# Kernel tuning notes

Hardware: AMD Instinct MI355X
Metric: run time of the kernel (lower is better)

## Reference

```python
import jax, jax.numpy as jnp
import numpy as np

B, L, C = 256, 256, 128
HID, H = 128, 4
D = HID // H            # 32
NUM_LAYERS = 2
NEG_SLOPE = 0.2
LN_EPS = 1e-5


def setup_inputs() -> dict:
    key = jax.random.key(0)
    ks = jax.random.split(key, 16)
    E = 4096
    x = jax.random.normal(ks[0], (B, L, C), dtype=jnp.float32)
    edge_index = jax.random.randint(ks[1], (2, E), 0, C, dtype=jnp.int64)
    s_in = 1.0 / np.sqrt(L)
    s_h = 1.0 / np.sqrt(HID)
    return {
        "x": x,
        "edge_index": edge_index,
        "emb_W": jax.random.normal(ks[2], (L, HID), jnp.float32) * s_in,
        "emb_b": jnp.zeros((HID,), jnp.float32),
        "lin_l_W": jax.random.normal(ks[3], (NUM_LAYERS, HID, HID), jnp.float32) * s_h,
        "lin_l_b": jnp.zeros((NUM_LAYERS, HID), jnp.float32),
        "lin_r_W": jax.random.normal(ks[4], (NUM_LAYERS, HID, HID), jnp.float32) * s_h,
        "lin_r_b": jnp.zeros((NUM_LAYERS, HID), jnp.float32),
        "att": jax.random.normal(ks[5], (NUM_LAYERS, H, D), jnp.float32) * (1.0 / np.sqrt(D)),
        "gat_bias": jnp.zeros((NUM_LAYERS, HID), jnp.float32),
        "ln_gamma": jnp.ones((NUM_LAYERS, HID), jnp.float32),
        "ln_beta": jnp.zeros((NUM_LAYERS, HID), jnp.float32),
        "proj_W": jax.random.normal(ks[6], (HID, L), jnp.float32) * s_h,
        "proj_b": jnp.zeros((L,), jnp.float32),
    }


def _batch_edges(edge_index):
    # replicate single-graph edges per batch sample with node offsets, then add self loops
    E = edge_index.shape[1]
    off = jnp.repeat(jnp.arange(B, dtype=edge_index.dtype) * C, E)
    src = jnp.tile(edge_index[0], B) + off
    dst = jnp.tile(edge_index[1], B) + off
    loop = jnp.arange(B * C, dtype=edge_index.dtype)
    return jnp.concatenate([src, loop]), jnp.concatenate([dst, loop])


def _layer_norm(x, g, b):
    mu = jnp.mean(x, axis=-1, keepdims=True)
    var = jnp.mean(jnp.square(x - mu), axis=-1, keepdims=True)
    return (x - mu) * jax.lax.rsqrt(var + LN_EPS) * g + b


def _gatv2(x, src, dst, Wl, bl, Wr, br, a, bias):
    N = x.shape[0]
    xl = (x @ Wl + bl).reshape(N, H, D)   # source-side transform
    xr = (x @ Wr + br).reshape(N, H, D)   # target-side transform
    e = jax.nn.leaky_relu(xl[src] + xr[dst], NEG_SLOPE)   # (E', H, D)
    logits = jnp.einsum('ehd,hd->eh', e, a)               # (E', H)
    m = jax.ops.segment_max(logits, dst, num_segments=N)
    p = jnp.exp(logits - m[dst])
    s = jax.ops.segment_sum(p, dst, num_segments=N)
    alpha = p / (s[dst] + 1e-16)
    out = jax.ops.segment_sum(xl[src] * alpha[:, :, None], dst, num_segments=N)
    return out.reshape(N, HID) + bias, alpha


def reference(x, edge_index, emb_W, emb_b, lin_l_W, lin_l_b, lin_r_W, lin_r_b,
              att, gat_bias, ln_gamma, ln_beta, proj_W, proj_b):
    src, dst = _batch_edges(edge_index)
    # (B, L, C) -> nodes are channels: (B*C, L) -> embed to HID
    h = x.transpose(0, 2, 1).reshape(B * C, L) @ emb_W + emb_b
    alpha = None
    for i in range(NUM_LAYERS):
        new_h, alpha = _gatv2(h, src, dst, lin_l_W[i], lin_l_b[i],
                              lin_r_W[i], lin_r_b[i], att[i], gat_bias[i])
        new_h = jax.nn.elu(new_h)
        h = h + new_h
        h = _layer_norm(h, ln_gamma[i], ln_beta[i])
        # dropout: eval mode, identity
    # attention map (to_dense_adj semantics: adj[b, src%C, dst%C] = mean_h(alpha), then transpose)
    b_idx = src // C
    dense = jnp.zeros((B, C, C), x.dtype).at[b_idx, src % C, dst % C].add(alpha.mean(axis=-1))
    attn_map = dense.transpose(0, 2, 1)
    out = (h @ proj_W + proj_b).reshape(B, C, L).transpose(0, 2, 1)  # (B, L, C)
    return out, attn_map
```

## Files before the change

### kernel.cpp

```cpp
#include <hip/hip_runtime.h>
#include <hip/hip_fp16.h>
#include <math.h>

#define BB 256
#define LL 256
#define CC 128
#define HIDD 128
#define HH 4
#define DD 32
#define EE 4096
#define NN (BB*CC)
#define NEG_SLOPE 0.2f
#define LN_EPS 1e-5f
#define DEGMAX 58
#define LOG2CAP 31
#define CSRSL 3840
#define ASLOT 4352
#define AEDGE 4224

typedef short bf16x8 __attribute__((ext_vector_type(8)));
typedef float f32x4 __attribute__((ext_vector_type(4)));

__device__ __forceinline__ float red64(float p) {
    p += __shfl_xor(p, 32);
    p += __shfl_xor(p, 16);
    p += __shfl_xor(p, 8);
    p += __shfl_xor(p, 4);
    p += __shfl_xor(p, 2);
    p += __shfl_xor(p, 1);
    return p;
}
__device__ __forceinline__ unsigned bfr(float f) {
    unsigned x = __float_as_uint(f);
    return (x + 0x7FFFu + ((x >> 16) & 1u)) >> 16;
}
__device__ __forceinline__ unsigned pack2(float a, float b) { return bfr(a) | (bfr(b) << 16); }
__device__ __forceinline__ float blo(unsigned u) { return __uint_as_float(u << 16); }
__device__ __forceinline__ float bhi(unsigned u) { return __uint_as_float(u & 0xFFFF0000u); }

__device__ __forceinline__ void stage_f32_rm(ushort* lds, const float* src, int ldm, int t) {
    #pragma unroll
    for (int i = 0; i < 8; ++i) {
        int flat = i*256 + t;
        int r = flat >> 4, c = flat & 15;
        const float* p = src + (size_t)r*ldm + c*8;
        float4 v0 = *(const float4*)p;
        float4 v1 = *(const float4*)(p + 4);
        uint4 pk;
        pk.x = pack2(v0.x, v0.y); pk.y = pack2(v0.z, v0.w);
        pk.z = pack2(v1.x, v1.y); pk.w = pack2(v1.z, v1.w);
        *(uint4*)&lds[((r*16) + (c ^ (r & 7)))*8] = pk;
    }
}
__device__ __forceinline__ void stage_bf16_rm(ushort* lds, const ushort* src, int ldm, int t) {
    #pragma unroll
    for (int i = 0; i < 8; ++i) {
        int flat = i*256 + t;
        int r = flat >> 4, c = flat & 15;
        uint4 pk = *(const uint4*)(src + (size_t)r*ldm + c*8);
        *(uint4*)&lds[((r*16) + (c ^ (r & 7)))*8] = pk;
    }
}
__device__ __forceinline__ void mfma_tile_128(const ushort* Als, const ushort* Bls,
                                              f32x4 acc[2][8], int w, int lane) {
    int mr = lane & 15, quad = lane >> 4;
    #pragma unroll
    for (int ks = 0; ks < 4; ++ks) {
        int ca = ks*4 + quad;
        bf16x8 a[2], b[8];
        #pragma unroll
        for (int mf = 0; mf < 2; ++mf) {
            int m = w*32 + mf*16 + mr;
            a[mf] = *(const bf16x8*)&Als[((m*16) + (ca ^ (m & 7)))*8];
        }
        #pragma unroll
        for (int nf = 0; nf < 8; ++nf) {
            int n = nf*16 + mr;
            b[nf] = *(const bf16x8*)&Bls[((n*16) + (ca ^ (n & 7)))*8];
        }
        #pragma unroll
        for (int mf = 0; mf < 2; ++mf)
            #pragma unroll
            for (int nf = 0; nf < 8; ++nf)
                acc[mf][nf] = __builtin_amdgcn_mfma_f32_16x16x32_bf16(a[mf], b[nf], acc[mf][nf], 0, 0, 0);
    }
}
#define ZERO_ACC(acc) { _Pragma("unroll") for (int i_=0;i_<2;++i_) { _Pragma("unroll") for (int j_=0;j_<8;++j_) acc[i_][j_] = (f32x4){0.f,0.f,0.f,0.f}; } }

__global__ __launch_bounds__(256) void prep_weights(const float* __restrict__ emb_W,
                                                    const float* __restrict__ lWl,
                                                    const float* __restrict__ lWr,
                                                    const float* __restrict__ pW,
                                                    ushort* __restrict__ WembT,
                                                    ushort* __restrict__ WlrT,
                                                    ushort* __restrict__ WpT) {
    int gid = blockIdx.x * 256 + threadIdx.x;
    float v[8];
    if (gid < 4096) {
        int f = gid >> 5, ch = gid & 31;
        #pragma unroll
        for (int j = 0; j < 8; ++j) v[j] = emb_W[(size_t)(ch*8 + j)*HIDD + f];
        uint4 pk; pk.x = pack2(v[0],v[1]); pk.y = pack2(v[2],v[3]);
        pk.z = pack2(v[4],v[5]); pk.w = pack2(v[6],v[7]);
        *(uint4*)&WembT[(size_t)f*LL + ch*8] = pk;
    } else if (gid < 12288) {
        int g = gid - 4096;
        int mat = g >> 11, f = (g >> 4) & 127, ch = g & 15;
        const float* src = ((mat & 1) ? lWr : lWl) + (size_t)(mat >> 1)*HIDD*HIDD;
        #pragma unroll
        for (int j = 0; j < 8; ++j) v[j] = src[(size_t)(ch*8 + j)*HIDD + f];
        uint4 pk; pk.x = pack2(v[0],v[1]); pk.y = pack2(v[2],v[3]);
        pk.z = pack2(v[4],v[5]); pk.w = pack2(v[6],v[7]);
        *(uint4*)&WlrT[(size_t)mat*HIDD*HIDD + (size_t)f*HIDD + ch*8] = pk;
    } else {
        int g = gid - 12288;
        int l = g >> 4, ch = g & 15;
        #pragma unroll
        for (int j = 0; j < 8; ++j) v[j] = pW[(size_t)(ch*8 + j)*LL + l];
        uint4 pk; pk.x = pack2(v[0],v[1]); pk.y = pack2(v[2],v[3]);
        pk.z = pack2(v[4],v[5]); pk.w = pack2(v[6],v[7]);
        *(uint4*)&WpT[(size_t)l*HIDD + ch*8] = pk;
    }
}

__global__ __launch_bounds__(256) void transpose_x(const float* __restrict__ x,
                                                   ushort* __restrict__ xbfT) {
    __shared__ float tile[CC][33];
    int b = blockIdx.y, l0 = blockIdx.x * 32;
    int t = threadIdx.x;
    #pragma unroll
    for (int i = 0; i < 4; ++i) {
        int flat = i*256 + t;
        int l = flat >> 5, c4 = flat & 31;
        float4 v = *(const float4*)&x[((size_t)b*LL + l0 + l)*CC + c4*4];
        tile[c4*4+0][l] = v.x; tile[c4*4+1][l] = v.y;
        tile[c4*4+2][l] = v.z; tile[c4*4+3][l] = v.w;
    }
    __syncthreads();
    #pragma unroll
    for (int i = 0; i < 2; ++i) {
        int flat = i*256 + t;
        int c = flat >> 2, ch = flat & 3;
        const float* p = &tile[c][ch*8];
        uint4 pk; pk.x = pack2(p[0],p[1]); pk.y = pack2(p[2],p[3]);
        pk.z = pack2(p[4],p[5]); pk.w = pack2(p[6],p[7]);
        *(uint4*)&xbfT[((size_t)b*CC + c)*LL + l0 + ch*8] = pk;
    }
}

__global__ __launch_bounds__(256) void build_csr(const int* __restrict__ edge,
                                                 int* __restrict__ csr_off,
                                                 int* __restrict__ csr_src) {
    __shared__ int cnt[CC];
    __shared__ int offs[CC+1];
    __shared__ int cur[CC];
    int t = threadIdx.x;
    if (t < CC) cnt[t] = 0;
    __syncthreads();
    for (int j = t; j < EE; j += 256) atomicAdd(&cnt[edge[EE + j]], 1);
    __syncthreads();
    if (t == 0) {
        int a = 0;
        for (int i = 0; i < CC; ++i) { offs[i] = a; a += cnt[i]; }
        offs[CC] = a;
    }
    __syncthreads();
    if (t < CC) cur[t] = offs[t];
    if (t <= CC) csr_off[t] = offs[t];
    __syncthreads();
    for (int j = t; j < EE; j += 256) {
        int pos = atomicAdd(&cur[edge[EE + j]], 1);
        csr_src[pos] = edge[j];
    }
}

__global__ __launch_bounds__(256) void embed_mfma(const ushort* __restrict__ xbfT,
                                                  const ushort* __restrict__ WembT,
                                                  const float* __restrict__ bias,
                                                  float* __restrict__ hout) {
    __shared__ __align__(16) ushort Als[128*16*8];
    __shared__ __align__(16) ushort Bls[128*16*8];
    int b = blockIdx.x;
    int t = threadIdx.x, lane = t & 63, w = t >> 6;
    f32x4 acc[2][8];
    ZERO_ACC(acc)
    #pragma unroll
    for (int kh = 0; kh < 2; ++kh) {
        if (kh) __syncthreads();
        stage_bf16_rm(Als, xbfT + (size_t)b*CC*LL + kh*128, LL, t);
        stage_bf16_rm(Bls, WembT + kh*128, LL, t);
        __syncthreads();
        mfma_tile_128(Als, Bls, acc, w, lane);
    }
    int mr = lane & 15, quad = lane >> 4;
    #pragma unroll
    for (int nf = 0; nf < 8; ++nf) {
        int f = nf*16 + mr;
        float bv = bias[f];
        #pragma unroll
        for (int mf = 0; mf < 2; ++mf)
            #pragma unroll
            for (int r = 0; r < 4; ++r) {
                int node = w*32 + mf*16 + quad*4 + r;
                hout[((size_t)b*CC + node)*HIDD + f] = acc[mf][nf][r] + bv;
            }
    }
}

__global__ __launch_bounds__(256) void lin_mfma(const float* __restrict__ hmat,
                                                const ushort* __restrict__ WlT,
                                                const ushort* __restrict__ WrT,
                                                const float* __restrict__ bl,
                                                const float* __restrict__ br,
                                                float* __restrict__ xlT,
                                                float* __restrict__ xrT) {
    __shared__ __align__(16) ushort Als[128*16*8];
    __shared__ __align__(16) ushort Bls[128*16*8];
    const ushort* W   = blockIdx.y ? WrT : WlT;
    const float* bias = blockIdx.y ? br : bl;
    float* out        = blockIdx.y ? xrT : xlT;
    int m0 = blockIdx.x * 128;
    int t = threadIdx.x, lane = t & 63, w = t >> 6;
    f32x4 acc[2][8];
    ZERO_ACC(acc)
    stage_f32_rm(Als, hmat + (size_t)m0*HIDD, HIDD, t);
    stage_bf16_rm(Bls, W, HIDD, t);
    __syncthreads();
    mfma_tile_128(Als, Bls, acc, w, lane);
    int mr = lane & 15, quad = lane >> 4;
    #pragma unroll
    for (int nf = 0; nf < 8; ++nf) {
        int f = nf*16 + mr;
        float bv = bias[f];
        int h = f >> 5, d = f & 31;
        #pragma unroll
        for (int mf = 0; mf < 2; ++mf)
            #pragma unroll
            for (int r = 0; r < 4; ++r) {
                int node = w*32 + mf*16 + quad*4 + r;
                out[(((size_t)blockIdx.x*HH + h)*CC + node)*DD + d] = acc[mf][nf][r] + bv;
            }
    }
}

__global__ __launch_bounds__(128) void gat_attn(const float* __restrict__ xlT,
                                                const float* __restrict__ xrT,
                                                const int* __restrict__ csr_off,
                                                const int* __restrict__ csr_src,
                                                const float* __restrict__ att,
                                                float* __restrict__ xagg,
                                                float* __restrict__ alpha_ws) {
    __shared__ __align__(16) uint2 xl4[8*129];
    __shared__ __half mylog[128*LOG2CAP];
    __shared__ unsigned char csr_s[CSRSL];
    int bid = blockIdx.x;
    int b = bid >> 3, h = (bid >> 1) & 3, half = bid & 1;
    int t = threadIdx.x;
    int dst = half*64 + (t >> 1), p = t & 1;

    const float* xl_g = xlT + ((size_t)b*HH + h)*CC*DD;
    #pragma unroll
    for (int i = 0; i < 8; ++i) {
        int flat = i*128 + t;
        int n = flat >> 3, c = flat & 7;
        float4 v = *(const float4*)&xl_g[(size_t)n*DD + c*4];
        xl4[c*129 + n] = make_uint2(pack2(v.x, v.y), pack2(v.z, v.w));
    }
    int rbase = csr_off[half*64];
    int rcnt  = csr_off[half*64 + 64] - rbase;
    if (rcnt > CSRSL) rcnt = CSRSL;
    for (int j = t; j < rcnt; j += 128)
        csr_s[j] = (unsigned char)csr_src[rbase + j];

    float att_r[32], r_r[32], q_r[32];
    const float* xr_g = xrT + (((size_t)b*HH + h)*CC + dst) * DD;
    #pragma unroll
    for (int c = 0; c < 8; ++c) {
        float4 xv = *(const float4*)&xr_g[c*4];
        float4 av = *(const float4*)&att[h*DD + c*4];
        att_r[c*4+0]=av.x; att_r[c*4+1]=av.y; att_r[c*4+2]=av.z; att_r[c*4+3]=av.w;
        r_r[c*4+0]=av.x*xv.x; r_r[c*4+1]=av.y*xv.y; r_r[c*4+2]=av.z*xv.z; r_r[c*4+3]=av.w*xv.w;
        q_r[c*4+0]=copysignf(0.4f,av.x); q_r[c*4+1]=copysignf(0.4f,av.y);
        q_r[c*4+2]=copysignf(0.4f,av.z); q_r[c*4+3]=copysignf(0.4f,av.w);
    }
    int base = csr_off[dst];
    int deg  = csr_off[dst+1] - base;
    if (deg > DEGMAX) deg = DEGMAX;
    int sbase = base - rbase;
    __syncthreads();

    __half* ml = &mylog[t*LOG2CAP];
    float m = -1e30f;
    int nv = 0;
    for (int vj = p; vj <= deg; vj += 2, ++nv) {
        int src = (vj < deg) ? (int)csr_s[sbase + vj] : dst;
        float a0=0.f, a1=0.f, a2=0.f, a3=0.f;
        #pragma unroll
        for (int q = 0; q < 8; ++q) {
            uint2 u = xl4[q*129 + src];
            float pp;
            pp = fmaf(att_r[4*q+0], blo(u.x), r_r[4*q+0]);
            a0 = fmaf(0.6f, pp, a0); a0 = fmaf(q_r[4*q+0], fabsf(pp), a0);
            pp = fmaf(att_r[4*q+1], bhi(u.x), r_r[4*q+1]);
            a1 = fmaf(0.6f, pp, a1); a1 = fmaf(q_r[4*q+1], fabsf(pp), a1);
            pp = fmaf(att_r[4*q+2], blo(u.y), r_r[4*q+2]);
            a2 = fmaf(0.6f, pp, a2); a2 = fmaf(q_r[4*q+2], fabsf(pp), a2);
            pp = fmaf(att_r[4*q+3], bhi(u.y), r_r[4*q+3]);
            a3 = fmaf(0.6f, pp, a3); a3 = fmaf(q_r[4*q+3], fabsf(pp), a3);
        }
        float l = (a0+a1) + (a2+a3);
        ml[nv] = __float2half(l);
        m = fmaxf(m, l);
    }
    m = fmaxf(m, __shfl_xor(m, 1));

    float s = 0.f;
    for (int k = 0; k < nv; ++k) {
        float e = __expf(__half2float(ml[k]) - m);
        s += e;
        ml[k] = __float2half(e);
    }
    s += __shfl_xor(s, 1);
    float is = 1.f / (s + 1e-16f);

    float acc_r[32];
    #pragma unroll
    for (int d = 0; d < 32; ++d) acc_r[d] = 0.f;
    float* aws = alpha_ws ? alpha_ws + (size_t)(b*HH + h)*ASLOT : nullptr;
    {
        int vj = p;
        for (int k = 0; k < nv; ++k, vj += 2) {
            int src = (vj < deg) ? (int)csr_s[sbase + vj] : dst;
            float alpha = __half2float(ml[k]) * is;
            if (aws) aws[(vj < deg) ? (base + vj) : (AEDGE + dst)] = alpha;
            #pragma unroll
            for (int q = 0; q < 8; ++q) {
                uint2 u = xl4[q*129 + src];
                acc_r[4*q+0] = fmaf(alpha, blo(u.x), acc_r[4*q+0]);
                acc_r[4*q+1] = fmaf(alpha, bhi(u.x), acc_r[4*q+1]);
                acc_r[4*q+2] = fmaf(alpha, blo(u.y), acc_r[4*q+2]);
                acc_r[4*q+3] = fmaf(alpha, bhi(u.y), acc_r[4*q+3]);
            }
        }
    }
    #pragma unroll
    for (int d = 0; d < 32; ++d) acc_r[d] += __shfl_xor(acc_r[d], 1);
    float* og = xagg + (((size_t)b*CC + dst)*HH + h) * DD + p*16;
    #pragma unroll
    for (int c = 0; c < 4; ++c) {
        float4 o = make_float4(acc_r[p*16+c*4+0], acc_r[p*16+c*4+1],
                               acc_r[p*16+c*4+2], acc_r[p*16+c*4+3]);
        *(float4*)&og[c*4] = o;
    }
}

__global__ __launch_bounds__(128) void gat_epilogue(const float* __restrict__ xagg,
                                                    const float* __restrict__ gbias,
                                                    const float* __restrict__ ln_g,
                                                    const float* __restrict__ ln_b,
                                                    const int* __restrict__ csr_off,
                                                    const int* __restrict__ csr_src,
                                                    const float* __restrict__ alpha_ws,
                                                    float* __restrict__ hmat,
                                                    float* __restrict__ attn_out) {
    __shared__ float attnrow[CC];
    __shared__ float wred[2], wred2[2];
    int node = blockIdx.x;
    int b = node >> 7, dstc = node & 127;
    int f = threadIdx.x;
    attnrow[f] = 0.f;

    float o = xagg[(size_t)node*HIDD + f] + gbias[f];
    o = o > 0.f ? o : (__expf(o) - 1.f);
    float hv = hmat[(size_t)node*HIDD + f] + o;

    float sum = red64(hv);
    if ((f & 63) == 0) wred[f >> 6] = sum;
    __syncthreads();
    float mean = (wred[0] + wred[1]) * 0.0078125f;
    float d = hv - mean;
    float q = red64(d * d);
    if ((f & 63) == 0) wred2[f >> 6] = q;
    __syncthreads();
    float var = (wred2[0] + wred2[1]) * 0.0078125f;
    hmat[(size_t)node*HIDD + f] = d * rsqrtf(var + LN_EPS) * ln_g[f] + ln_b[f];

    if (attn_out) {
        int base = csr_off[dstc];
        int deg  = csr_off[dstc+1] - base;
        if (deg > DEGMAX) deg = DEGMAX;
        for (int j = f; j < deg; j += 128) {
            float a = 0.f;
            #pragma unroll
            for (int hh = 0; hh < HH; ++hh)
                a += alpha_ws[(size_t)(b*HH + hh)*ASLOT + base + j];
            atomicAdd(&attnrow[csr_src[base + j]], 0.25f * a);
        }
        if (f == 0) {
            float a = 0.f;
            #pragma unroll
            for (int hh = 0; hh < HH; ++hh)
                a += alpha_ws[(size_t)(b*HH + hh)*ASLOT + AEDGE + dstc];
            atomicAdd(&attnrow[dstc], 0.25f * a);
        }
        __syncthreads();
        attn_out[(size_t)node*CC + f] = attnrow[f];
    }
}

__global__ __launch_bounds__(256) void proj_mfma(const float* __restrict__ hmat,
                                                 const ushort* __restrict__ WpT,
                                                 const float* __restrict__ bias,
                                                 float* __restrict__ out) {
    __shared__ __align__(16) ushort Als[128*16*8];
    __shared__ __align__(16) ushort Bls[128*16*8];
    int l0 = blockIdx.x * 128;
    int b  = blockIdx.y;
    int t = threadIdx.x, lane = t & 63, w = t >> 6;
    f32x4 acc[2][8];
    ZERO_ACC(acc)
    stage_bf16_rm(Als, WpT + (size_t)l0*HIDD, HIDD, t);
    stage_f32_rm(Bls, hmat + (size_t)b*CC*HIDD, HIDD, t);
    __syncthreads();
    mfma_tile_128(Als, Bls, acc, w, lane);
    int mr = lane & 15, quad = lane >> 4;
    #pragma unroll
    for (int nf = 0; nf < 8; ++nf) {
        int c = nf*16 + mr;
        #pragma unroll
        for (int mf = 0; mf < 2; ++mf)
            #pragma unroll
            for (int r = 0; r < 4; ++r) {
                int l = l0 + w*32 + mf*16 + quad*4 + r;
                out[((size_t)b*LL + l)*CC + c] = acc[mf][nf][r] + bias[l];
            }
    }
}

extern "C" void kernel_launch(void* const* d_in, const int* in_sizes, int n_in,
                              void* d_out, int out_size, void* d_ws, size_t ws_size,
                              hipStream_t stream) {
    const float* x        = (const float*)d_in[0];
    const int*   edge     = (const int*)d_in[1];
    const float* emb_W    = (const float*)d_in[2];
    const float* emb_b    = (const float*)d_in[3];
    const float* lin_l_W  = (const float*)d_in[4];
    const float* lin_l_b  = (const float*)d_in[5];
    const float* lin_r_W  = (const float*)d_in[6];
    const float* lin_r_b  = (const float*)d_in[7];
    const float* att      = (const float*)d_in[8];
    const float* gat_bias = (const float*)d_in[9];
    const float* ln_g     = (const float*)d_in[10];
    const float* ln_b     = (const float*)d_in[11];
    const float* proj_W   = (const float*)d_in[12];
    const float* proj_b   = (const float*)d_in[13];

    float* h     = (float*)d_ws;
    float* xlT   = h    + (size_t)NN * HIDD;
    float* xrT   = xlT  + (size_t)NN * HIDD;
    float* xagg  = xrT  + (size_t)NN * HIDD;
    float* shared_region = xagg + (size_t)NN * HIDD;
    float*  alpha = shared_region;
    ushort* xbfT  = (ushort*)shared_region;
    ushort* WembT = (ushort*)(shared_region + (size_t)BB*HH*ASLOT);
    ushort* WlrT  = WembT + (size_t)CC*LL;
    ushort* WpT   = WlrT + (size_t)4*HIDD*HIDD;
    int* csr_off  = (int*)(WpT + (size_t)LL*HIDD);
    int* csr_src  = csr_off + 132;

    float* out0 = (float*)d_out;
    float* attn = out0 + (size_t)BB * LL * CC;

    build_csr<<<1, 256, 0, stream>>>(edge, csr_off, csr_src);
    prep_weights<<<64, 256, 0, stream>>>(emb_W, lin_l_W, lin_r_W, proj_W, WembT, WlrT, WpT);
    transpose_x<<<dim3(8, BB), 256, 0, stream>>>(x, xbfT);
    embed_mfma<<<BB, 256, 0, stream>>>(xbfT, WembT, emb_b, h);
    for (int layer = 0; layer < 2; ++layer) {
        float* aws = (layer == 1) ? alpha : nullptr;
        lin_mfma<<<dim3(NN/128, 2), 256, 0, stream>>>(h,
            WlrT + (size_t)(layer*2 + 0)*HIDD*HIDD,
            WlrT + (size_t)(layer*2 + 1)*HIDD*HIDD,
            lin_l_b + layer*HIDD, lin_r_b + layer*HIDD,
            xlT, xrT);
        gat_attn<<<BB*HH*2, 128, 0, stream>>>(xlT, xrT, csr_off, csr_src,
            att + layer*HIDD, xagg, aws);
        gat_epilogue<<<NN, 128, 0, stream>>>(xagg,
            gat_bias + layer*HIDD, ln_g + layer*HIDD, ln_b + layer*HIDD,
            csr_off, csr_src, aws, h, (layer == 1) ? attn : nullptr);
    }
    proj_mfma<<<dim3(2, BB), 256, 0, stream>>>(h, WpT, proj_b, out0);
}
```

Baseline: 313.9 us.

## Use packed fp16 math in GAT attention and split leaky-relu logit algebraically

Switches the staged source features in the attention kernel from bf16 to fp16 and does the logit and aggregation arithmetic with packed half2 FMAs. The leaky-relu logit is rewritten as 0.6·a·(xl+xr) + 0.4·a·|xl+xr|. The linear part is precomputed once per node (Slq in shared memory) and once per destination (Srq), so each edge evaluates only the abs term. This halves per-edge ALU work but accumulates attention logits and weighted sums in fp16, which costs accuracy and adds an extra barrier.

Result: faster. 307.7 us (-2.0%).

```diff
diff --git a/kernel.cpp b/kernel.cpp
--- a/kernel.cpp
+++ b/kernel.cpp
@@ -35,8 +35,8 @@
     return (x + 0x7FFFu + ((x >> 16) & 1u)) >> 16;
 }
 __device__ __forceinline__ unsigned pack2(float a, float b) { return bfr(a) | (bfr(b) << 16); }
-__device__ __forceinline__ float blo(unsigned u) { return __uint_as_float(u << 16); }
-__device__ __forceinline__ float bhi(unsigned u) { return __uint_as_float(u & 0xFFFF0000u); }
+__device__ __forceinline__ __half2 u2h(unsigned u) { __half2 r; *(unsigned*)&r = u; return r; }
+__device__ __forceinline__ unsigned h2u(__half2 h) { return *(unsigned*)&h; }
 
 __device__ __forceinline__ void stage_f32_rm(ushort* lds, const float* src, int ldm, int t) {
     #pragma unroll
@@ -251,6 +251,7 @@
                                                 float* __restrict__ xagg,
                                                 float* __restrict__ alpha_ws) {
     __shared__ __align__(16) uint2 xl4[8*129];
+    __shared__ float Slq[128];
     __shared__ __half mylog[128*LOG2CAP];
     __shared__ unsigned char csr_s[CSRSL];
     int bid = blockIdx.x;
@@ -264,7 +265,9 @@
         int flat = i*128 + t;
         int n = flat >> 3, c = flat & 7;
         float4 v = *(const float4*)&xl_g[(size_t)n*DD + c*4];
-        xl4[c*129 + n] = make_uint2(pack2(v.x, v.y), pack2(v.z, v.w));
+        __half2 lo = __floats2half2_rn(v.x, v.y);
+        __half2 hi = __floats2half2_rn(v.z, v.w);
+        xl4[c*129 + n] = make_uint2(h2u(lo), h2u(hi));
     }
     int rbase = csr_off[half*64];
     int rcnt  = csr_off[half*64 + 64] - rbase;
@@ -272,21 +275,36 @@
     for (int j = t; j < rcnt; j += 128)
         csr_s[j] = (unsigned char)csr_src[rbase + j];
 
-    float att_r[32], r_r[32], q_r[32];
+    __half2 qa2[16], xr2[16];
+    float Srq = 0.f;
     const float* xr_g = xrT + (((size_t)b*HH + h)*CC + dst) * DD;
     #pragma unroll
     for (int c = 0; c < 8; ++c) {
         float4 xv = *(const float4*)&xr_g[c*4];
         float4 av = *(const float4*)&att[h*DD + c*4];
-        att_r[c*4+0]=av.x; att_r[c*4+1]=av.y; att_r[c*4+2]=av.z; att_r[c*4+3]=av.w;
-        r_r[c*4+0]=av.x*xv.x; r_r[c*4+1]=av.y*xv.y; r_r[c*4+2]=av.z*xv.z; r_r[c*4+3]=av.w*xv.w;
-        q_r[c*4+0]=copysignf(0.4f,av.x); q_r[c*4+1]=copysignf(0.4f,av.y);
-        q_r[c*4+2]=copysignf(0.4f,av.z); q_r[c*4+3]=copysignf(0.4f,av.w);
+        xr2[2*c+0] = __floats2half2_rn(xv.x, xv.y);
+        xr2[2*c+1] = __floats2half2_rn(xv.z, xv.w);
+        qa2[2*c+0] = __floats2half2_rn(0.4f*av.x, 0.4f*av.y);
+        qa2[2*c+1] = __floats2half2_rn(0.4f*av.z, 0.4f*av.w);
+        Srq += 0.4f*(av.x*xv.x + av.y*xv.y + av.z*xv.z + av.w*xv.w);
     }
     int base = csr_off[dst];
     int deg  = csr_off[dst+1] - base;
     if (deg > DEGMAX) deg = DEGMAX;
     int sbase = base - rbase;
+    __syncthreads();
+
+    {
+        __half2 s0 = __floats2half2_rn(0.f, 0.f), s1 = s0;
+        #pragma unroll
+        for (int q = 0; q < 8; ++q) {
+            uint2 u = xl4[q*129 + t];
+            s0 = __hfma2(qa2[2*q+0], u2h(u.x), s0);
+            s1 = __hfma2(qa2[2*q+1], u2h(u.y), s1);
+        }
+        __half2 ss = __hadd2(s0, s1);
+        Slq[t] = __low2float(ss) + __high2float(ss);
+    }
     __syncthreads();
 
     __half* ml = &mylog[t*LOG2CAP];
@@ -294,21 +312,23 @@
     int nv = 0;
     for (int vj = p; vj <= deg; vj += 2, ++nv) {
         int src = (vj < deg) ? (int)csr_s[sbase + vj] : dst;
-        float a0=0.f, a1=0.f, a2=0.f, a3=0.f;
+        __half2 t0 = __floats2half2_rn(0.f, 0.f), t1 = t0, t2 = t0, t3 = t0;
         #pragma unroll
         for (int q = 0; q < 8; ++q) {
             uint2 u = xl4[q*129 + src];
-            float pp;
-            pp = fmaf(att_r[4*q+0], blo(u.x), r_r[4*q+0]);
-            a0 = fmaf(0.6f, pp, a0); a0 = fmaf(q_r[4*q+0], fabsf(pp), a0);
-            pp = fmaf(att_r[4*q+1], bhi(u.x), r_r[4*q+1]);
-            a1 = fmaf(0.6f, pp, a1); a1 = fmaf(q_r[4*q+1], fabsf(pp), a1);
-            pp = fmaf(att_r[4*q+2], blo(u.y), r_r[4*q+2]);
-            a2 = fmaf(0.6f, pp, a2); a2 = fmaf(q_r[4*q+2], fabsf(pp), a2);
-            pp = fmaf(att_r[4*q+3], bhi(u.y), r_r[4*q+3]);
-            a3 = fmaf(0.6f, pp, a3); a3 = fmaf(q_r[4*q+3], fabsf(pp), a3);
-        }
-        float l = (a0+a1) + (a2+a3);
+            __half2 w0 = __hadd2(u2h(u.x), xr2[2*q+0]);
+            __half2 w1 = __hadd2(u2h(u.y), xr2[2*q+1]);
+            if (q & 1) {
+                t2 = __hfma2(qa2[2*q+0], __habs2(w0), t2);
+                t3 = __hfma2(qa2[2*q+1], __habs2(w1), t3);
+            } else {
+                t0 = __hfma2(qa2[2*q+0], __habs2(w0), t0);
+                t1 = __hfma2(qa2[2*q+1], __habs2(w1), t1);
+            }
+        }
+        __half2 ts = __hadd2(__hadd2(t0, t1), __hadd2(t2, t3));
+        float T = __low2float(ts) + __high2float(ts);
+        float l = fmaf(1.5f, Slq[src] + Srq, T);
         ml[nv] = __float2half(l);
         m = fmaxf(m, l);
     }
@@ -323,9 +343,9 @@
     s += __shfl_xor(s, 1);
     float is = 1.f / (s + 1e-16f);
 
-    float acc_r[32];
-    #pragma unroll
-    for (int d = 0; d < 32; ++d) acc_r[d] = 0.f;
+    __half2 acc2[16];
+    #pragma unroll
+    for (int q = 0; q < 16; ++q) acc2[q] = __floats2half2_rn(0.f, 0.f);
     float* aws = alpha_ws ? alpha_ws + (size_t)(b*HH + h)*ASLOT : nullptr;
     {
         int vj = p;
@@ -333,23 +353,26 @@
             int src = (vj < deg) ? (int)csr_s[sbase + vj] : dst;
             float alpha = __half2float(ml[k]) * is;
             if (aws) aws[(vj < deg) ? (base + vj) : (AEDGE + dst)] = alpha;
+            __half2 al2 = __float2half2_rn(alpha);
             #pragma unroll
             for (int q = 0; q < 8; ++q) {
                 uint2 u = xl4[q*129 + src];
-                acc_r[4*q+0] = fmaf(alpha, blo(u.x), acc_r[4*q+0]);
-                acc_r[4*q+1] = fmaf(alpha, bhi(u.x), acc_r[4*q+1]);
-                acc_r[4*q+2] = fmaf(alpha, blo(u.y), acc_r[4*q+2]);
-                acc_r[4*q+3] = fmaf(alpha, bhi(u.y), acc_r[4*q+3]);
+                acc2[2*q+0] = __hfma2(al2, u2h(u.x), acc2[2*q+0]);
+                acc2[2*q+1] = __hfma2(al2, u2h(u.y), acc2[2*q+1]);
             }
         }
     }
     #pragma unroll
-    for (int d = 0; d < 32; ++d) acc_r[d] += __shfl_xor(acc_r[d], 1);
+    for (int q = 0; q < 16; ++q) {
+        unsigned ob = __shfl_xor(h2u(acc2[q]), 1);
+        acc2[q] = __hadd2(acc2[q], u2h(ob));
+    }
     float* og = xagg + (((size_t)b*CC + dst)*HH + h) * DD + p*16;
     #pragma unroll
     for (int c = 0; c < 4; ++c) {
-        float4 o = make_float4(acc_r[p*16+c*4+0], acc_r[p*16+c*4+1],
-                               acc_r[p*16+c*4+2], acc_r[p*16+c*4+3]);
+        __half2 e0 = acc2[p*8 + 2*c], e1 = acc2[p*8 + 2*c + 1];
+        float4 o = make_float4(__low2float(e0), __high2float(e0),
+                               __low2float(e1), __high2float(e1));
         *(float4*)&og[c*4] = o;
     }
 }
```
